# Kernel optimization log

Hardware: AMD Instinct MI355X
Metric: run time of the kernel (lower is better)

Reference implementation:

```python
import jax, jax.numpy as jnp
import numpy as np

HEADS = 16
HEAD_DIM = 64


def _attn(q, k, v):
    # q: [..., Q, h, d], k/v: [..., K, h, d]  (non-causal SDPA, scale 1/sqrt(d))
    scale = 1.0 / np.sqrt(HEAD_DIM).astype(np.float32)
    s = jnp.einsum('...qhd,...khd->...hqk', q, k) * scale
    p = jax.nn.softmax(s, axis=-1)
    return jnp.einsum('...hqk,...khd->...qhd', p, v)


def setup_inputs() -> dict:
    key = jax.random.key(0)
    k0, k1, k2 = jax.random.split(key, 3)
    B, T, H, W, D = 4, 32, 16, 16, 1024
    inner = HEADS * HEAD_DIM
    x = jax.random.normal(k0, (B, T, H, W, D), jnp.float32)
    Wqkv = jax.random.normal(k1, (D, 3 * inner), jnp.float32) / np.sqrt(D)
    Wout = jax.random.normal(k2, (inner, D), jnp.float32) / np.sqrt(inner)
    bout = jnp.zeros((D,), jnp.float32)
    return {"x": x, "Wqkv": Wqkv, "Wout": Wout, "bout": bout, "reference_length": 3}


def reference(x, Wqkv, Wout, bout, reference_length):
    B, T, H, W, D = x.shape
    length = reference_length + 1
    n = T // length            # n_frames (chunks)
    S = H * W                  # tokens per frame
    h, d = HEADS, HEAD_DIM

    qkv = jnp.einsum('bthwD,De->bthwe', x, Wqkv)
    q, k, v = jnp.split(qkv, 3, axis=-1)

    def rs(t):  # -> [B, n, length, S, h, d]
        return t.reshape(B, n, length, S, h, d)

    qr, kr, vr = rs(q), rs(k), rs(v)

    # non-last chunks: query = first frame of chunk, keys/values = remaining r frames
    q_pre = qr[:, :-1, 0]                                             # [B, n-1, S, h, d]
    k_pre = kr[:, :-1, 1:].reshape(B, n - 1, reference_length * S, h, d)
    v_pre = vr[:, :-1, 1:].reshape(B, n - 1, reference_length * S, h, d)
    o_pre = _attn(q_pre, k_pre, v_pre).reshape(B, n - 1, H, W, h * d)

    # last chunk: all `length` frames are queries, keys/values = frames 1..length-1
    q_last = qr[:, -1].reshape(B, length * S, h, d)
    k_last = kr[:, -1, 1:].reshape(B, reference_length * S, h, d)
    v_last = vr[:, -1, 1:].reshape(B, reference_length * S, h, d)
    o_last = _attn(q_last, k_last, v_last).reshape(B, length, H, W, h * d)

    o = jnp.concatenate([o_pre, o_last], axis=1)  # [B, n-1+length, H, W, inner]
    return jnp.einsum('bthwe,eD->bthwD', o, Wout) + bout
```

## Files before the change

kernel.cpp:

```cpp
#include <hip/hip_runtime.h>
#include <hip/hip_bf16.h>

typedef __bf16 bf16;
typedef __bf16 bf16x8 __attribute__((ext_vector_type(8)));
typedef float  f32x4  __attribute__((ext_vector_type(4)));
typedef float  f32x4v __attribute__((ext_vector_type(4)));
typedef unsigned int u32x4 __attribute__((ext_vector_type(4)));
typedef unsigned short u16x4 __attribute__((ext_vector_type(4)));

#define DEV __device__ __forceinline__

DEV void gload_lds16(const bf16* g, bf16* l) {
    __builtin_amdgcn_global_load_lds(
        (__attribute__((address_space(1))) void*)g,
        (__attribute__((address_space(3))) void*)l, 16, 0, 0);
}

DEV bf16x8 as_bf(u32x4 v) { return __builtin_bit_cast(bf16x8, v); }

DEV f32x4 mfma16(bf16x8 a, bf16x8 b, f32x4 c) {
    return __builtin_amdgcn_mfma_f32_16x16x32_bf16(a, b, c, 0, 0, 0);
}

DEV int cvtpk(float lo, float hi) {
    int r;
    asm("v_cvt_pk_bf16_f32 %0, %1, %2" : "=v"(r) : "v"(lo), "v"(hi));
    return r;
}

constexpr int D_   = 1024;
constexpr int S_   = 256;
constexpr int TOUT = 11;
constexpr int MQ   = 4 * TOUT * S_;
constexpr int MKV  = 4 * 8 * 3 * S_;
constexpr int KVL  = 768;

constexpr int PB_WQKV = 768;
constexpr int PB_WOUT = 256;
constexpr int PB_GQ   = MQ  * 128 / 256;
constexpr int PB_GKV  = MKV * 128 / 256;
constexpr int PB_TOT  = PB_WQKV + PB_WOUT + PB_GQ + PB_GKV;

__global__ void prep(const float* __restrict__ x,
                     const float* __restrict__ Wqkv,
                     const float* __restrict__ Wout,
                     bf16* __restrict__ Aq, bf16* __restrict__ Akv,
                     bf16* __restrict__ Wqkv_t, bf16* __restrict__ Wout_t)
{
    __shared__ float T[64][65];
    const int tid = threadIdx.x;
    int wg = blockIdx.x;

    if (wg < PB_WQKV + PB_WOUT) {
        const float* W; bf16* Wt; int N, bid2;
        if (wg < PB_WQKV) { W = Wqkv; Wt = Wqkv_t; N = 3072; bid2 = wg; }
        else              { W = Wout; Wt = Wout_t; N = 1024; bid2 = wg - PB_WQKV; }
        const int kt = bid2 & 15, nt = bid2 >> 4;
        const int k0 = kt * 64, n0 = nt * 64;
        for (int i = 0; i < 16; ++i) {
            const int e = i * 256 + tid;
            const int kk = e >> 6, nn = e & 63;
            T[nn][kk] = W[(size_t)(k0 + kk) * N + n0 + nn];
        }
        __syncthreads();
        for (int i = 0; i < 16; ++i) {
            const int e = i * 256 + tid;
            const int n = e >> 6, kk = e & 63;
            Wt[(size_t)(n0 + n) * 1024 + k0 + kk] = (bf16)T[n][kk];
        }
        return;
    }
    wg -= PB_WQKV + PB_WOUT;

    int row, part;
    const float* src;
    bf16* dst;
    if (wg < PB_GQ) {
        const int idx = wg * 256 + tid;
        row = idx >> 7; part = idx & 127;
        const int b    = row / (TOUT * S_);
        const int r2   = row - b * (TOUT * S_);
        const int tout = r2 >> 8;
        const int s    = r2 & 255;
        const int tx   = tout < 7 ? tout * 4 : 28 + (tout - 7);
        src = x + ((size_t)((b * 32 + tx) * S_ + s)) * D_ + part * 8;
        dst = Aq + (size_t)row * D_ + part * 8;
    } else {
        const int idx = (wg - PB_GQ) * 256 + tid;
        row = idx >> 7; part = idx & 127;
        const int b  = row / 6144;
        const int r2 = row - b * 6144;
        const int c  = r2 / KVL;
        const int j  = r2 - c * KVL;
        const int f  = 1 + (j >> 8);
        const int s  = j & 255;
        const int tx = c * 4 + f;
        src = x + ((size_t)((b * 32 + tx) * S_ + s)) * D_ + part * 8;
        dst = Akv + (size_t)row * D_ + part * 8;
    }
    f32x4v v0 = *(const f32x4v*)src;
    f32x4v v1 = *(const f32x4v*)(src + 4);
    bf16x8 o;
    o[0]=(bf16)v0[0]; o[1]=(bf16)v0[1]; o[2]=(bf16)v0[2]; o[3]=(bf16)v0[3];
    o[4]=(bf16)v1[0]; o[5]=(bf16)v1[1]; o[6]=(bf16)v1[2]; o[7]=(bf16)v1[3];
    *(bf16x8*)dst = o;
}

#define PH_BEGIN() do { \
    __builtin_amdgcn_s_barrier(); \
    asm volatile("s_waitcnt lgkmcnt(0)" ::: "memory"); \
    __builtin_amdgcn_sched_barrier(0); \
    __builtin_amdgcn_s_setprio(1); \
} while(0)

#define PH_MMEND() do { \
    __builtin_amdgcn_s_setprio(0); \
    __builtin_amdgcn_sched_barrier(0); \
} while(0)

#define PH_CLOSE4() do { \
    asm volatile("s_waitcnt vmcnt(4)" ::: "memory"); \
    __builtin_amdgcn_s_barrier(); \
} while(0)

#define STAGE_A(bufc, half, tile) do { \
    const bf16* s0_ = pA + (size_t)(half) * 64 * 1024 + (tile) * 64; \
    bf16* d0_ = ldsA + (bufc) * 16384 + (half) * 8192; \
    gload_lds16(s0_, d0_); \
    gload_lds16(s0_ + (size_t)128 * 1024, d0_ + 4096); \
} while(0)

#define STAGE_B(bufc, half, tile) do { \
    const bf16* s0_ = pB + (size_t)(half) * 32 * 1024 + (tile) * 64; \
    bf16* d0_ = ldsB + (bufc) * 16384 + (half) * 8192; \
    gload_lds16(s0_, d0_); \
    gload_lds16(s0_ + (size_t)128 * 1024, d0_ + 4096); \
} while(0)

#define LDAJ(dst, bufc, mh, J) do { \
    const bf16* p_ = sm + (bufc) * 16384 + (mh) * 8192 + (J) * 1024; \
    dst[J][0] = *(const u32x4*)(p_ + eA0); \
    dst[J][1] = *(const u32x4*)(p_ + eA1); \
} while(0)

#define LDBH(dst, bufc, nh) do { \
    const bf16* p_ = sm + 32768 + (bufc) * 16384 + (nh) * 8192; \
    dst[0][0] = *(const u32x4*)(p_ + eB0); \
    dst[0][1] = *(const u32x4*)(p_ + eB1); \
    dst[1][0] = *(const u32x4*)(p_ + 1024 + eB0); \
    dst[1][1] = *(const u32x4*)(p_ + 1024 + eB1); \
} while(0)

#define MMX(av, bv, mh, nh) do { \
    _Pragma("unroll") \
    for (int j_ = 0; j_ < 4; ++j_) { \
        _Pragma("unroll") \
        for (int i_ = 0; i_ < 2; ++i_) { \
            f32x4 c_ = acc[(mh)*4 + j_][(nh)*2 + i_]; \
            c_ = mfma16(as_bf(av[j_][0]), as_bf(bv[i_][0]), c_); \
            c_ = mfma16(as_bf(av[j_][1]), as_bf(bv[i_][1]), c_); \
            acc[(mh)*4 + j_][(nh)*2 + i_] = c_; \
        } \
    } \
} while(0)

#define GEMM_MAINLOOP() do { \
    STAGE_A(0, 0, 0); STAGE_A(0, 1, 0); STAGE_B(0, 0, 0); STAGE_B(0, 1, 0); \
    STAGE_A(1, 0, 1); STAGE_B(1, 0, 1); STAGE_B(1, 1, 1); \
    asm volatile("s_waitcnt vmcnt(0)" ::: "memory"); \
    __builtin_amdgcn_s_barrier(); \
    LDAJ(aX,0,0,0); LDAJ(aX,0,0,1); LDAJ(aX,0,0,2); LDAJ(aX,0,0,3); \
    LDBH(bP0,0,0); LDBH(bQ0,0,1); \
    _Pragma("unroll 1") \
    for (int t = 0; t < 8; ++t) { \
        const int T1 = 2 * t + 1; \
        const int n0 = (2 * t + 2 < 15) ? 2 * t + 2 : 15; \
        const int n1 = (2 * t + 3 < 15) ? 2 * t + 3 : 15; \
        STAGE_A(1, 1, T1); STAGE_B(0, 0, n0); \
        PH_BEGIN(); MMX(aX, bP0, 0, 0); MMX(aX, bQ0, 0, 1); PH_MMEND(); \
        LDAJ(aY, 0, 1, 0); LDAJ(aY, 0, 1, 1); LDAJ(aY, 0, 1, 2); LDAJ(aY, 0, 1, 3); \
        LDBH(bP1, 1, 0); \
        PH_CLOSE4(); \
        STAGE_A(0, 0, n0); STAGE_B(0, 1, n0); \
        PH_BEGIN(); MMX(aY, bP0, 1, 0); MMX(aY, bQ0, 1, 1); PH_MMEND(); \
        LDAJ(aX, 1, 0, 0); LDAJ(aX, 1, 0, 1); LDAJ(aX, 1, 0, 2); LDAJ(aX, 1, 0, 3); \
        LDBH(bQ1, 1, 1); \
        PH_CLOSE4(); \
        STAGE_A(0, 1, n0); STAGE_B(1, 0, n1); \
        PH_BEGIN(); MMX(aX, bP1, 0, 0); MMX(aX, bQ1, 0, 1); PH_MMEND(); \
        LDAJ(aY, 1, 1, 0); LDAJ(aY, 1, 1, 1); LDAJ(aY, 1, 1, 2); LDAJ(aY, 1, 1, 3); \
        LDBH(bP0, 0, 0); \
        PH_CLOSE4(); \
        STAGE_A(1, 0, n1); STAGE_B(1, 1, n1); \
        PH_BEGIN(); MMX(aY, bP1, 1, 0); MMX(aY, bQ1, 1, 1); PH_MMEND(); \
        LDAJ(aX, 0, 0, 0); LDAJ(aX, 0, 0, 1); LDAJ(aX, 0, 0, 2); LDAJ(aX, 0, 0, 3); \
        LDBH(bQ0, 0, 1); \
        PH_CLOSE4(); \
    } \
    asm volatile("s_waitcnt vmcnt(0) lgkmcnt(0)" ::: "memory"); \
} while(0)

#define GEMM_PREAMBLE() \
    const int wr = wid >> 2, wc = wid & 3; \
    const int l15 = lane & 15, l4 = lane >> 4; \
    const int Rrow = (wid << 3) + (lane >> 3); \
    const int G    = (lane & 7) ^ (lane >> 3); \
    const bf16* pA = A  + (size_t)(bm * 256 + Rrow) * 1024 + G * 8; \
    const int wc1 = Rrow >> 5, cc1 = Rrow & 31; \
    const bf16* pB = Bt + (size_t)(bn * 256 + wc1 * 64 + cc1) * 1024 + G * 8; \
    bf16* ldsA = sm + (wid << 9); \
    bf16* ldsB = sm + 32768 + (wid << 9); \
    const int g0  = l4 ^ (l15 & 7); \
    const int eA0 = wr * 4096 + l15 * 64 + g0 * 8; \
    const int eA1 = eA0 ^ 32; \
    const int eB0 = wc * 2048 + l15 * 64 + g0 * 8; \
    const int eB1 = eB0 ^ 32; \
    f32x4 acc[8][4]; \
    u32x4 aX[4][2], aY[4][2], bP0[2][2], bQ0[2][2], bP1[2][2], bQ1[2][2]; \
    { const f32x4 zf_ = {0.f, 0.f, 0.f, 0.f}; \
      _Pragma("unroll") \
      for (int m_ = 0; m_ < 8; ++m_) \
          _Pragma("unroll") \
          for (int n_ = 0; n_ < 4; ++n_) acc[m_][n_] = zf_; }

__global__ __launch_bounds__(512, 2) void gemm_qkv(
    const bf16* __restrict__ Aq, const bf16* __restrict__ Akv,
    const bf16* __restrict__ Wt,
    bf16* __restrict__ Qb, bf16* __restrict__ Kb, bf16* __restrict__ Vt)
{
    __shared__ bf16 sm[65536];
    const int tid = threadIdx.x, lane = tid & 63, wid = tid >> 6;

    int wg = blockIdx.x;
    {
        const int xcd = wg & 7, off = wg >> 3;
        wg = xcd * 118 + off;
    }
    const bool isQ = wg < 176;
    const bf16* A;  const bf16* Bt;  int bm, bn;
    if (isQ) {
        const int sg = wg >> 4, s = wg & 15;
        bm = sg * 4 + (s >> 2);
        bn = s & 3;
        A = Aq;  Bt = Wt;
    } else {
        const int id2 = wg - 176;
        const int sg = id2 >> 4, s = id2 & 15;
        bm = (sg % 24) * 4 + (s >> 2);
        bn = (sg / 24) * 4 + (s & 3);
        A = Akv; Bt = Wt + (size_t)1024 * 1024;
    }

    GEMM_PREAMBLE();
    GEMM_MAINLOOP();

    if (isQ || bn < 4) {
        bf16* C = isQ ? Qb : Kb;
        #pragma unroll
        for (int m = 0; m < 8; ++m) {
            const int row = bm * 256 + wr * 128 + m * 16 + l4 * 4;
            #pragma unroll
            for (int n = 0; n < 4; ++n) {
                const int col = bn * 256 + wc * 64 + n * 16 + l15;
                f32x4 v = acc[m][n];
                #pragma unroll
                for (int r = 0; r < 4; ++r)
                    C[(size_t)(row + r) * 1024 + col] = (bf16)v[r];
            }
        }
    } else {
        const int vb = bm / 3;
        const int j0base = (bm % 3) * 256;
        #pragma unroll
        for (int m = 0; m < 8; ++m) {
            const int j0 = j0base + wr * 128 + m * 16 + l4 * 4;
            #pragma unroll
            for (int n = 0; n < 4; ++n) {
                const int colv = (bn - 4) * 256 + wc * 64 + n * 16 + l15;
                f32x4 v = acc[m][n];
                u16x4 pk;
                #pragma unroll
                for (int r = 0; r < 4; ++r) {
                    bf16 t = (bf16)v[r];
                    pk[r] = __builtin_bit_cast(unsigned short, t);
                }
                *(u16x4*)(Vt + ((size_t)vb * 1024 + colv) * KVL + j0) = pk;
            }
        }
    }
}

__global__ __launch_bounds__(512, 2) void gemm_out(
    const bf16* __restrict__ A, const bf16* __restrict__ Bt,
    float* __restrict__ Cf, const float* __restrict__ bias)
{
    __shared__ bf16 sm[65536];
    const int tid = threadIdx.x, lane = tid & 63, wid = tid >> 6;

    int wg = blockIdx.x;
    {
        const int xcd = wg & 7, off = wg >> 3;
        wg = xcd * 22 + off;
    }
    const int sg = wg >> 4, s = wg & 15;
    const int bm = sg * 4 + (s >> 2), bn = s & 3;

    GEMM_PREAMBLE();
    GEMM_MAINLOOP();

    #pragma unroll
    for (int m = 0; m < 8; ++m) {
        const int row = bm * 256 + wr * 128 + m * 16 + l4 * 4;
        #pragma unroll
        for (int n = 0; n < 4; ++n) {
            const int col = bn * 256 + wc * 64 + n * 16 + l15;
            f32x4 v = acc[m][n];
            const float bs = bias[col];
            #pragma unroll
            for (int r = 0; r < 4; ++r)
                Cf[(size_t)(row + r) * 1024 + col] = v[r] + bs;
        }
    }
}

__global__ __launch_bounds__(256, 4) void attn_fwd(
    const bf16* __restrict__ Q, const bf16* __restrict__ K,
    const bf16* __restrict__ Vt, bf16* __restrict__ O)
{
    __shared__ bf16 Kl[2][2][64][32];
    __shared__ bf16 Vl[2][2][64][32];

    const int tid = threadIdx.x, lane = tid & 63, wid = tid >> 6;
    int bid = blockIdx.x;
    const int h = bid & 15; bid >>= 4;
    const int qt = bid % 44, b = bid / 44;
    const int chunk = qt < 28 ? (qt >> 2) : 7;
    const int qrow0 = b * (TOUT * S_) +
                      (qt < 28 ? chunk * S_ + (qt & 3) * 64 : 7 * S_ + (qt - 28) * 64);

    const bf16* kg = K  + ((size_t)(b * 8 + chunk) * KVL) * 1024 + h * 64;
    const bf16* vg = Vt + ((size_t)((b * 8 + chunk) * 16 + h)) * 64 * KVL;

    const int l15 = lane & 15, l4 = lane >> 4;

    const bf16* qp = Q + (size_t)(qrow0 + wid * 16 + l15) * D_ + h * 64 + l4 * 8;
    u32x4 q0, q1;
    {
        bf16x8 t0 = *(const bf16x8*)qp;
        bf16x8 t1 = *(const bf16x8*)(qp + 32);
        #pragma unroll
        for (int j = 0; j < 8; ++j) {
            t0[j] = (bf16)((float)t0[j] * 0.125f);
            t1[j] = (bf16)((float)t1[j] * 0.125f);
        }
        q0 = __builtin_bit_cast(u32x4, t0);
        q1 = __builtin_bit_cast(u32x4, t1);
    }

    const int R   = wid * 16 + (lane >> 2);
    const int gsw = ((lane & 3) ^ ((lane >> 3) & 3)) * 8;
    const int rg  = (l4 ^ ((l15 >> 1) & 3)) * 8;

    const int baseA = ((2 * (l4 & 1)) * 16 + l15) * 4;
    const int baseB = baseA + 64;
    const bool hi2 = (l4 & 2) != 0;

    float m_s = -1e30f, l_s = 0.f;
    f32x4 oacc[4];
    const f32x4 zf = {0.f, 0.f, 0.f, 0.f};
    #pragma unroll
    for (int m2 = 0; m2 < 4; ++m2) oacc[m2] = zf;

#define ASTAGE(c, t) do { \
    const int kv0_ = (t) * 64; \
    gload_lds16(kg + (size_t)(kv0_ + R) * 1024 + gsw,      &Kl[c][0][0][0] + wid * 512); \
    gload_lds16(kg + (size_t)(kv0_ + R) * 1024 + 32 + gsw, &Kl[c][1][0][0] + wid * 512); \
    gload_lds16(vg + (size_t)R * KVL + kv0_ + gsw,         &Vl[c][0][0][0] + wid * 512); \
    gload_lds16(vg + (size_t)R * KVL + kv0_ + 32 + gsw,    &Vl[c][1][0][0] + wid * 512); \
} while (0)

    ASTAGE(0, 0);
    __syncthreads();

    #pragma unroll 1
    for (int kt = 0; kt < 12; ++kt) {
        const int cur = kt & 1;
        if (kt < 11) ASTAGE(cur ^ 1, kt + 1);

        f32x4 s[4];
        #pragma unroll
        for (int n = 0; n < 4; ++n) {
            const bf16* kp = &Kl[cur][0][n * 16 + l15][0] + rg;
            const u32x4 k0 = *(const u32x4*)kp;
            const u32x4 k1 = *(const u32x4*)(kp + 2048);
            f32x4 t = mfma16(as_bf(k0), as_bf(q0), zf);
            s[n] = mfma16(as_bf(k1), as_bf(q1), t);
        }

        float pm = s[0][0];
        #pragma unroll
        for (int n = 0; n < 4; ++n)
            #pragma unroll
            for (int r = 0; r < 4; ++r) pm = fmaxf(pm, s[n][r]);
        pm = fmaxf(pm, __shfl_xor(pm, 16));
        pm = fmaxf(pm, __shfl_xor(pm, 32));
        const float mn = fmaxf(m_s, pm);
        const float al = __expf(m_s - mn);
        m_s = mn;
        float p[4][4];
        float sum = 0.f;
        #pragma unroll
        for (int n = 0; n < 4; ++n)
            #pragma unroll
            for (int r = 0; r < 4; ++r) {
                const float e = __expf(s[n][r] - mn);
                p[n][r] = e; sum += e;
            }
        sum += __shfl_xor(sum, 16);
        sum += __shfl_xor(sum, 32);
        l_s = l_s * al + sum;
        #pragma unroll
        for (int m2 = 0; m2 < 4; ++m2) oacc[m2] *= al;

        int u[4][2];
        #pragma unroll
        for (int n = 0; n < 4; ++n) {
            u[n][0] = cvtpk(p[n][0], p[n][1]);
            u[n][1] = cvtpk(p[n][2], p[n][3]);
        }

        #pragma unroll
        for (int kk = 0; kk < 2; ++kk) {
            const int e0 = __builtin_amdgcn_ds_bpermute(baseA, u[2 * kk][0]);
            const int f0 = __builtin_amdgcn_ds_bpermute(baseA, u[2 * kk + 1][0]);
            const int e1 = __builtin_amdgcn_ds_bpermute(baseA, u[2 * kk][1]);
            const int f1 = __builtin_amdgcn_ds_bpermute(baseA, u[2 * kk + 1][1]);
            const int e2 = __builtin_amdgcn_ds_bpermute(baseB, u[2 * kk][0]);
            const int f2 = __builtin_amdgcn_ds_bpermute(baseB, u[2 * kk + 1][0]);
            const int e3 = __builtin_amdgcn_ds_bpermute(baseB, u[2 * kk][1]);
            const int f3 = __builtin_amdgcn_ds_bpermute(baseB, u[2 * kk + 1][1]);
            u32x4 pb;
            pb[0] = (unsigned)(hi2 ? f0 : e0);
            pb[1] = (unsigned)(hi2 ? f1 : e1);
            pb[2] = (unsigned)(hi2 ? f2 : e2);
            pb[3] = (unsigned)(hi2 ? f3 : e3);
            #pragma unroll
            for (int m2 = 0; m2 < 4; ++m2) {
                const u32x4 vf = *(const u32x4*)(&Vl[cur][kk][m2 * 16 + l15][0] + rg);
                oacc[m2] = mfma16(as_bf(vf), as_bf(pb), oacc[m2]);
            }
        }
        __syncthreads();
    }
#undef ASTAGE

    const float inv = 1.f / l_s;
    bf16* sc = &Kl[0][0][0][0] + wid * 1152;
    #pragma unroll
    for (int m2 = 0; m2 < 4; ++m2)
        #pragma unroll
        for (int r = 0; r < 4; ++r)
            sc[l15 * 72 + m2 * 16 + l4 * 4 + r] = (bf16)(oacc[m2][r] * inv);
    const int rq = lane >> 2, rd = (lane & 3) * 16;
    const bf16* sr = sc + rq * 72 + rd;
    const u32x4 o0 = *(const u32x4*)sr;
    const u32x4 o1 = *(const u32x4*)(sr + 8);
    bf16* op = O + (size_t)(qrow0 + wid * 16 + rq) * D_ + h * 64 + rd;
    *(u32x4*)op = o0;
    *(u32x4*)(op + 8) = o1;
}

extern "C" void kernel_launch(void* const* d_in, const int* in_sizes, int n_in,
                              void* d_out, int out_size, void* d_ws, size_t ws_size,
                              hipStream_t stream) {
    (void)in_sizes; (void)n_in; (void)out_size; (void)ws_size;
    const float* x    = (const float*)d_in[0];
    const float* Wqkv = (const float*)d_in[1];
    const float* Wout = (const float*)d_in[2];
    const float* bout = (const float*)d_in[3];

    bf16* Aq     = (bf16*)d_ws;
    bf16* Akv    = Aq     + (size_t)MQ  * 1024;
    bf16* Wqkv_t = Akv    + (size_t)MKV * 1024;
    bf16* Wout_t = Wqkv_t + (size_t)3072 * 1024;
    bf16* Qb     = Wout_t + (size_t)1024 * 1024;
    bf16* Kb     = Qb     + (size_t)MQ  * 1024;
    bf16* Vtb    = Kb     + (size_t)MKV * 1024;
    bf16* Ob     = Aq;

    prep<<<PB_TOT, 256, 0, stream>>>(x, Wqkv, Wout, Aq, Akv, Wqkv_t, Wout_t);

    gemm_qkv<<<944, 512, 0, stream>>>(Aq, Akv, Wqkv_t, Qb, Kb, Vtb);

    attn_fwd<<<4 * 44 * 16, 256, 0, stream>>>(Qb, Kb, Vtb, Ob);

    gemm_out<<<176, 512, 0, stream>>>(Ob, Wout_t, (float*)d_out, bout);
}
```

Measured before the change: 285.1 us.

## Fuse fp32-to-bf16 activation gather into QKV GEMM A-operand loading

Removes the separate prep pass that gathered the x frames and converted them to bf16 into staging buffers. gemm_qkv now reads fp32 x directly, converts it in registers and writes bf16 tiles to LDS. The main loop is restructured into eight finer phases with a single set of B fragment registers and new vmcnt waits, and gemm_out gets the same reworked pipeline. This saves a full read and write of the activation matrix, at the cost of twice the global A traffic per GEMM tile plus extra VGPRs and conversion work inside the GEMM.

```diff
diff --git a/kernel.cpp b/kernel.cpp
--- a/kernel.cpp
+++ b/kernel.cpp
@@ -37,73 +37,31 @@
 
 constexpr int PB_WQKV = 768;
 constexpr int PB_WOUT = 256;
-constexpr int PB_GQ   = MQ  * 128 / 256;
-constexpr int PB_GKV  = MKV * 128 / 256;
-constexpr int PB_TOT  = PB_WQKV + PB_WOUT + PB_GQ + PB_GKV;
-
-__global__ void prep(const float* __restrict__ x,
-                     const float* __restrict__ Wqkv,
+
+__global__ void prep(const float* __restrict__ Wqkv,
                      const float* __restrict__ Wout,
-                     bf16* __restrict__ Aq, bf16* __restrict__ Akv,
                      bf16* __restrict__ Wqkv_t, bf16* __restrict__ Wout_t)
 {
     __shared__ float T[64][65];
     const int tid = threadIdx.x;
     int wg = blockIdx.x;
 
-    if (wg < PB_WQKV + PB_WOUT) {
-        const float* W; bf16* Wt; int N, bid2;
-        if (wg < PB_WQKV) { W = Wqkv; Wt = Wqkv_t; N = 3072; bid2 = wg; }
-        else              { W = Wout; Wt = Wout_t; N = 1024; bid2 = wg - PB_WQKV; }
-        const int kt = bid2 & 15, nt = bid2 >> 4;
-        const int k0 = kt * 64, n0 = nt * 64;
-        for (int i = 0; i < 16; ++i) {
-            const int e = i * 256 + tid;
-            const int kk = e >> 6, nn = e & 63;
-            T[nn][kk] = W[(size_t)(k0 + kk) * N + n0 + nn];
-        }
-        __syncthreads();
-        for (int i = 0; i < 16; ++i) {
-            const int e = i * 256 + tid;
-            const int n = e >> 6, kk = e & 63;
-            Wt[(size_t)(n0 + n) * 1024 + k0 + kk] = (bf16)T[n][kk];
-        }
-        return;
-    }
-    wg -= PB_WQKV + PB_WOUT;
-
-    int row, part;
-    const float* src;
-    bf16* dst;
-    if (wg < PB_GQ) {
-        const int idx = wg * 256 + tid;
-        row = idx >> 7; part = idx & 127;
-        const int b    = row / (TOUT * S_);
-        const int r2   = row - b * (TOUT * S_);
-        const int tout = r2 >> 8;
-        const int s    = r2 & 255;
-        const int tx   = tout < 7 ? tout * 4 : 28 + (tout - 7);
-        src = x + ((size_t)((b * 32 + tx) * S_ + s)) * D_ + part * 8;
-        dst = Aq + (size_t)row * D_ + part * 8;
-    } else {
-        const int idx = (wg - PB_GQ) * 256 + tid;
-        row = idx >> 7; part = idx & 127;
-        const int b  = row / 6144;
-        const int r2 = row - b * 6144;
-        const int c  = r2 / KVL;
-        const int j  = r2 - c * KVL;
-        const int f  = 1 + (j >> 8);
-        const int s  = j & 255;
-        const int tx = c * 4 + f;
-        src = x + ((size_t)((b * 32 + tx) * S_ + s)) * D_ + part * 8;
-        dst = Akv + (size_t)row * D_ + part * 8;
-    }
-    f32x4v v0 = *(const f32x4v*)src;
-    f32x4v v1 = *(const f32x4v*)(src + 4);
-    bf16x8 o;
-    o[0]=(bf16)v0[0]; o[1]=(bf16)v0[1]; o[2]=(bf16)v0[2]; o[3]=(bf16)v0[3];
-    o[4]=(bf16)v1[0]; o[5]=(bf16)v1[1]; o[6]=(bf16)v1[2]; o[7]=(bf16)v1[3];
-    *(bf16x8*)dst = o;
+    const float* W; bf16* Wt; int N, bid2;
+    if (wg < PB_WQKV) { W = Wqkv; Wt = Wqkv_t; N = 3072; bid2 = wg; }
+    else              { W = Wout; Wt = Wout_t; N = 1024; bid2 = wg - PB_WQKV; }
+    const int kt = bid2 & 15, nt = bid2 >> 4;
+    const int k0 = kt * 64, n0 = nt * 64;
+    for (int i = 0; i < 16; ++i) {
+        const int e = i * 256 + tid;
+        const int kk = e >> 6, nn = e & 63;
+        T[nn][kk] = W[(size_t)(k0 + kk) * N + n0 + nn];
+    }
+    __syncthreads();
+    for (int i = 0; i < 16; ++i) {
+        const int e = i * 256 + tid;
+        const int n = e >> 6, kk = e & 63;
+        Wt[(size_t)(n0 + n) * 1024 + k0 + kk] = (bf16)T[n][kk];
+    }
 }
 
 #define PH_BEGIN() do { \
@@ -118,8 +76,13 @@
     __builtin_amdgcn_sched_barrier(0); \
 } while(0)
 
-#define PH_CLOSE4() do { \
-    asm volatile("s_waitcnt vmcnt(4)" ::: "memory"); \
+#define PH_CLOSE() do { \
+    asm volatile("s_waitcnt vmcnt(6)" ::: "memory"); \
+    __builtin_amdgcn_s_barrier(); \
+} while(0)
+
+#define XCLOSE() do { \
+    asm volatile("s_waitcnt vmcnt(12)" ::: "memory"); \
     __builtin_amdgcn_s_barrier(); \
 } while(0)
 
@@ -135,6 +98,25 @@
     bf16* d0_ = ldsB + (bufc) * 16384 + (half) * 8192; \
     gload_lds16(s0_, d0_); \
     gload_lds16(s0_ + (size_t)128 * 1024, d0_ + 4096); \
+} while(0)
+
+#define ALD(set, half, tile) do { \
+    const float* s_ = px + (size_t)(half) * 65536 + (tile) * 64; \
+    set##0 = *(const f32x4v*)s_; \
+    set##1 = *(const f32x4v*)(s_ + 4); \
+    set##2 = *(const f32x4v*)(s_ + 131072); \
+    set##3 = *(const f32x4v*)(s_ + 131072 + 4); \
+} while(0)
+
+#define AWR(set, bufc, half) do { \
+    bf16* d_ = ldsA + (bufc) * 16384 + (half) * 8192 + lane * 8; \
+    bf16x8 o0_, o1_; \
+    o0_[0]=(bf16)set##0[0]; o0_[1]=(bf16)set##0[1]; o0_[2]=(bf16)set##0[2]; o0_[3]=(bf16)set##0[3]; \
+    o0_[4]=(bf16)set##1[0]; o0_[5]=(bf16)set##1[1]; o0_[6]=(bf16)set##1[2]; o0_[7]=(bf16)set##1[3]; \
+    o1_[0]=(bf16)set##2[0]; o1_[1]=(bf16)set##2[1]; o1_[2]=(bf16)set##2[2]; o1_[3]=(bf16)set##2[3]; \
+    o1_[4]=(bf16)set##3[0]; o1_[5]=(bf16)set##3[1]; o1_[6]=(bf16)set##3[2]; o1_[7]=(bf16)set##3[3]; \
+    *(bf16x8*)d_ = o0_; \
+    *(bf16x8*)(d_ + 4096) = o1_; \
 } while(0)
 
 #define LDAJ(dst, bufc, mh, J) do { \
@@ -164,48 +146,20 @@
     } \
 } while(0)
 
-#define GEMM_MAINLOOP() do { \
-    STAGE_A(0, 0, 0); STAGE_A(0, 1, 0); STAGE_B(0, 0, 0); STAGE_B(0, 1, 0); \
-    STAGE_A(1, 0, 1); STAGE_B(1, 0, 1); STAGE_B(1, 1, 1); \
-    asm volatile("s_waitcnt vmcnt(0)" ::: "memory"); \
-    __builtin_amdgcn_s_barrier(); \
-    LDAJ(aX,0,0,0); LDAJ(aX,0,0,1); LDAJ(aX,0,0,2); LDAJ(aX,0,0,3); \
-    LDBH(bP0,0,0); LDBH(bQ0,0,1); \
-    _Pragma("unroll 1") \
-    for (int t = 0; t < 8; ++t) { \
-        const int T1 = 2 * t + 1; \
-        const int n0 = (2 * t + 2 < 15) ? 2 * t + 2 : 15; \
-        const int n1 = (2 * t + 3 < 15) ? 2 * t + 3 : 15; \
-        STAGE_A(1, 1, T1); STAGE_B(0, 0, n0); \
-        PH_BEGIN(); MMX(aX, bP0, 0, 0); MMX(aX, bQ0, 0, 1); PH_MMEND(); \
-        LDAJ(aY, 0, 1, 0); LDAJ(aY, 0, 1, 1); LDAJ(aY, 0, 1, 2); LDAJ(aY, 0, 1, 3); \
-        LDBH(bP1, 1, 0); \
-        PH_CLOSE4(); \
-        STAGE_A(0, 0, n0); STAGE_B(0, 1, n0); \
-        PH_BEGIN(); MMX(aY, bP0, 1, 0); MMX(aY, bQ0, 1, 1); PH_MMEND(); \
-        LDAJ(aX, 1, 0, 0); LDAJ(aX, 1, 0, 1); LDAJ(aX, 1, 0, 2); LDAJ(aX, 1, 0, 3); \
-        LDBH(bQ1, 1, 1); \
-        PH_CLOSE4(); \
-        STAGE_A(0, 1, n0); STAGE_B(1, 0, n1); \
-        PH_BEGIN(); MMX(aX, bP1, 0, 0); MMX(aX, bQ1, 0, 1); PH_MMEND(); \
-        LDAJ(aY, 1, 1, 0); LDAJ(aY, 1, 1, 1); LDAJ(aY, 1, 1, 2); LDAJ(aY, 1, 1, 3); \
-        LDBH(bP0, 0, 0); \
-        PH_CLOSE4(); \
-        STAGE_A(1, 0, n1); STAGE_B(1, 1, n1); \
-        PH_BEGIN(); MMX(aY, bP1, 1, 0); MMX(aY, bQ1, 1, 1); PH_MMEND(); \
-        LDAJ(aX, 0, 0, 0); LDAJ(aX, 0, 0, 1); LDAJ(aX, 0, 0, 2); LDAJ(aX, 0, 0, 3); \
-        LDBH(bQ0, 0, 1); \
-        PH_CLOSE4(); \
-    } \
-    asm volatile("s_waitcnt vmcnt(0) lgkmcnt(0)" ::: "memory"); \
-} while(0)
-
-#define GEMM_PREAMBLE() \
+#define GEMM_REGS() \
+    f32x4 acc[8][4]; \
+    u32x4 aX[4][2], aY[4][2], bP[2][2], bQ[2][2]; \
+    { const f32x4 zf_ = {0.f, 0.f, 0.f, 0.f}; \
+      _Pragma("unroll") \
+      for (int m_ = 0; m_ < 8; ++m_) \
+          _Pragma("unroll") \
+          for (int n_ = 0; n_ < 4; ++n_) acc[m_][n_] = zf_; }
+
+#define GEMM_ADDR() \
     const int wr = wid >> 2, wc = wid & 3; \
     const int l15 = lane & 15, l4 = lane >> 4; \
     const int Rrow = (wid << 3) + (lane >> 3); \
     const int G    = (lane & 7) ^ (lane >> 3); \
-    const bf16* pA = A  + (size_t)(bm * 256 + Rrow) * 1024 + G * 8; \
     const int wc1 = Rrow >> 5, cc1 = Rrow & 31; \
     const bf16* pB = Bt + (size_t)(bn * 256 + wc1 * 64 + cc1) * 1024 + G * 8; \
     bf16* ldsA = sm + (wid << 9); \
@@ -214,18 +168,10 @@
     const int eA0 = wr * 4096 + l15 * 64 + g0 * 8; \
     const int eA1 = eA0 ^ 32; \
     const int eB0 = wc * 2048 + l15 * 64 + g0 * 8; \
-    const int eB1 = eB0 ^ 32; \
-    f32x4 acc[8][4]; \
-    u32x4 aX[4][2], aY[4][2], bP0[2][2], bQ0[2][2], bP1[2][2], bQ1[2][2]; \
-    { const f32x4 zf_ = {0.f, 0.f, 0.f, 0.f}; \
-      _Pragma("unroll") \
-      for (int m_ = 0; m_ < 8; ++m_) \
-          _Pragma("unroll") \
-          for (int n_ = 0; n_ < 4; ++n_) acc[m_][n_] = zf_; }
+    const int eB1 = eB0 ^ 32;
 
 __global__ __launch_bounds__(512, 2) void gemm_qkv(
-    const bf16* __restrict__ Aq, const bf16* __restrict__ Akv,
-    const bf16* __restrict__ Wt,
+    const float* __restrict__ x, const bf16* __restrict__ Wt,
     bf16* __restrict__ Qb, bf16* __restrict__ Kb, bf16* __restrict__ Vt)
 {
     __shared__ bf16 sm[65536];
@@ -237,22 +183,79 @@
         wg = xcd * 118 + off;
     }
     const bool isQ = wg < 176;
-    const bf16* A;  const bf16* Bt;  int bm, bn;
+    const bf16* Bt;  int bm, bn, xrow;
     if (isQ) {
         const int sg = wg >> 4, s = wg & 15;
-        bm = sg * 4 + (s >> 2);
-        bn = s & 3;
-        A = Aq;  Bt = Wt;
+        bm = sg * 4 + (s >> 2); bn = s & 3;
+        Bt = Wt;
+        const int b = bm / 11, tout = bm % 11;
+        const int tx = tout < 7 ? tout * 4 : 28 + (tout - 7);
+        xrow = (b * 32 + tx) * 256;
     } else {
         const int id2 = wg - 176;
-        const int sg = id2 >> 4, s = id2 & 15;
-        bm = (sg % 24) * 4 + (s >> 2);
-        bn = (sg / 24) * 4 + (s & 3);
-        A = Akv; Bt = Wt + (size_t)1024 * 1024;
-    }
-
-    GEMM_PREAMBLE();
-    GEMM_MAINLOOP();
+        const int sg = id2 >> 5, s = id2 & 31;
+        bm = sg * 4 + (s >> 3); bn = s & 7;
+        Bt = Wt + (size_t)1024 * 1024;
+        const int b = bm / 24, r2 = bm % 24, c = r2 / 3, part = r2 % 3;
+        const int tx = c * 4 + 1 + part;
+        xrow = (b * 32 + tx) * 256;
+    }
+
+    GEMM_ADDR();
+    const float* px = x + (size_t)(xrow + Rrow) * 1024 + G * 8;
+    GEMM_REGS();
+    f32x4v sX0, sX1, sX2, sX3, sY0, sY1, sY2, sY3;
+
+    ALD(sX, 0, 0);
+    ALD(sY, 1, 0);
+    STAGE_B(0, 0, 0); STAGE_B(0, 1, 0); STAGE_B(1, 0, 1); STAGE_B(1, 1, 1);
+    AWR(sX, 0, 0); AWR(sY, 0, 1);
+    ALD(sX, 0, 1);
+    AWR(sX, 1, 0);
+    ALD(sY, 1, 1);
+    asm volatile("s_waitcnt lgkmcnt(0)" ::: "memory");
+    __builtin_amdgcn_s_barrier();
+    LDAJ(aX,0,0,0); LDAJ(aX,0,0,1); LDAJ(aX,0,0,2); LDAJ(aX,0,0,3);
+    LDBH(bP,0,0);
+
+    #pragma unroll 1
+    for (int t = 0; t < 8; ++t) {
+        const int n0 = (2 * t + 2 < 15) ? 2 * t + 2 : 15;
+        const int n1 = (2 * t + 3 < 15) ? 2 * t + 3 : 15;
+        ALD(sX, 0, n0); AWR(sY, 1, 1);
+        PH_BEGIN(); MMX(aX, bP, 0, 0); PH_MMEND();
+        LDBH(bQ, 0, 1); LDAJ(aY, 0, 1, 0);
+        XCLOSE();
+        ALD(sY, 1, n0); AWR(sX, 0, 0);
+        PH_BEGIN(); MMX(aX, bQ, 0, 1); PH_MMEND();
+        LDAJ(aY, 0, 1, 1); LDAJ(aY, 0, 1, 2); LDAJ(aY, 0, 1, 3);
+        XCLOSE();
+        STAGE_B(0, 0, n0);
+        PH_BEGIN(); MMX(aY, bP, 1, 0); PH_MMEND();
+        LDAJ(aX, 1, 0, 0); LDAJ(aX, 1, 0, 1); LDAJ(aX, 1, 0, 2);
+        XCLOSE();
+        STAGE_B(0, 1, n0);
+        PH_BEGIN(); MMX(aY, bQ, 1, 1); PH_MMEND();
+        LDAJ(aX, 1, 0, 3); LDBH(bP, 1, 0);
+        XCLOSE();
+        ALD(sX, 0, n1); AWR(sY, 0, 1);
+        PH_BEGIN(); MMX(aX, bP, 0, 0); PH_MMEND();
+        LDBH(bQ, 1, 1); LDAJ(aY, 1, 1, 0);
+        XCLOSE();
+        ALD(sY, 1, n1); AWR(sX, 1, 0);
+        PH_BEGIN(); MMX(aX, bQ, 0, 1); PH_MMEND();
+        LDAJ(aY, 1, 1, 1); LDAJ(aY, 1, 1, 2); LDAJ(aY, 1, 1, 3);
+        XCLOSE();
+        STAGE_B(1, 0, n1);
+        PH_BEGIN(); MMX(aY, bP, 1, 0); PH_MMEND();
+        LDAJ(aX, 0, 0, 0); LDAJ(aX, 0, 0, 1); LDAJ(aX, 0, 0, 2);
+        XCLOSE();
+        STAGE_B(1, 1, n1);
+        PH_BEGIN(); MMX(aY, bQ, 1, 1); PH_MMEND();
+        LDAJ(aX, 0, 0, 3); LDBH(bP, 0, 0);
+        XCLOSE();
+    }
+    asm volatile("s_waitcnt vmcnt(0) lgkmcnt(0)" ::: "memory");
 
     if (isQ || bn < 4) {
         bf16* C = isQ ? Qb : Kb;
@@ -281,8 +284,8 @@
                 u16x4 pk;
                 #pragma unroll
                 for (int r = 0; r < 4; ++r) {
-                    bf16 t = (bf16)v[r];
-                    pk[r] = __builtin_bit_cast(unsigned short, t);
+                    bf16 tt = (bf16)v[r];
+                    pk[r] = __builtin_bit_cast(unsigned short, tt);
                 }
                 *(u16x4*)(Vt + ((size_t)vb * 1024 + colv) * KVL + j0) = pk;
             }
@@ -305,8 +308,55 @@
     const int sg = wg >> 4, s = wg & 15;
     const int bm = sg * 4 + (s >> 2), bn = s & 3;
 
-    GEMM_PREAMBLE();
-    GEMM_MAINLOOP();
+    GEMM_ADDR();
+    const bf16* pA = A + (size_t)(bm * 256 + Rrow) * 1024 + G * 8;
+    GEMM_REGS();
+
+    STAGE_A(0, 0, 0); STAGE_A(0, 1, 0); STAGE_B(0, 0, 0); STAGE_B(0, 1, 0);
+    STAGE_A(1, 0, 1); STAGE_B(1, 0, 1); STAGE_B(1, 1, 1);
+    asm volatile("s_waitcnt vmcnt(6)" ::: "memory");
+    __builtin_amdgcn_s_barrier();
+    LDAJ(aX,0,0,0); LDAJ(aX,0,0,1); LDAJ(aX,0,0,2); LDAJ(aX,0,0,3);
+    LDBH(bP,0,0);
+    #pragma unroll 1
+    for (int t = 0; t < 8; ++t) {
+        const int T1 = 2 * t + 1;
+        const int n0 = (2 * t + 2 < 15) ? 2 * t + 2 : 15;
+        const int n1 = (2 * t + 3 < 15) ? 2 * t + 3 : 15;
+        STAGE_A(1, 1, T1);
+        PH_BEGIN(); MMX(aX, bP, 0, 0); PH_MMEND();
+        LDBH(bQ, 0, 1); LDAJ(aY, 0, 1, 0);
+        PH_CLOSE();
+        STAGE_A(0, 0, n0);
+        PH_BEGIN(); MMX(aX, bQ, 0, 1); PH_MMEND();
+        LDAJ(aY, 0, 1, 1); LDAJ(aY, 0, 1, 2); LDAJ(aY, 0, 1, 3);
+        PH_CLOSE();
+        STAGE_B(0, 0, n0);
+        PH_BEGIN(); MMX(aY, bP, 1, 0); PH_MMEND();
+        LDAJ(aX, 1, 0, 0); LDAJ(aX, 1, 0, 1); LDAJ(aX, 1, 0, 2);
+        PH_CLOSE();
+        STAGE_B(0, 1, n0);
+        PH_BEGIN(); MMX(aY, bQ, 1, 1); PH_MMEND();
+        LDAJ(aX, 1, 0, 3); LDBH(bP, 1, 0);
+        PH_CLOSE();
+        STAGE_A(0, 1, n0);
+        PH_BEGIN(); MMX(aX, bP, 0, 0); PH_MMEND();
+        LDBH(bQ, 1, 1); LDAJ(aY, 1, 1, 0);
+        PH_CLOSE();
+        STAGE_A(1, 0, n1);
+        PH_BEGIN(); MMX(aX, bQ, 0, 1); PH_MMEND();
+        LDAJ(aY, 1, 1, 1); LDAJ(aY, 1, 1, 2); LDAJ(aY, 1, 1, 3);
+        PH_CLOSE();
+        STAGE_B(1, 0, n1);
+        PH_BEGIN(); MMX(aY, bP, 1, 0); PH_MMEND();
+        LDAJ(aX, 0, 0, 0); LDAJ(aX, 0, 0, 1); LDAJ(aX, 0, 0, 2);
+        PH_CLOSE();
+        STAGE_B(1, 1, n1);
+        PH_BEGIN(); MMX(aY, bQ, 1, 1); PH_MMEND();
+        LDAJ(aX, 0, 0, 3); LDBH(bP, 0, 0);
+        PH_CLOSE();
+    }
+    asm volatile("s_waitcnt vmcnt(0) lgkmcnt(0)" ::: "memory");
 
     #pragma unroll
     for (int m = 0; m < 8; ++m) {
@@ -479,18 +529,16 @@
     const float* Wout = (const float*)d_in[2];
     const float* bout = (const float*)d_in[3];
 
-    bf16* Aq     = (bf16*)d_ws;
-    bf16* Akv    = Aq     + (size_t)MQ  * 1024;
-    bf16* Wqkv_t = Akv    + (size_t)MKV * 1024;
+    bf16* Ob     = (bf16*)d_ws;
+    bf16* Wqkv_t = Ob     + (size_t)(MQ + MKV) * 1024;
     bf16* Wout_t = Wqkv_t + (size_t)3072 * 1024;
     bf16* Qb     = Wout_t + (size_t)1024 * 1024;
     bf16* Kb     = Qb     + (size_t)MQ  * 1024;
     bf16* Vtb    = Kb     + (size_t)MKV * 1024;
-    bf16* Ob     = Aq;
-
-    prep<<<PB_TOT, 256, 0, stream>>>(x, Wqkv, Wout, Aq, Akv, Wqkv_t, Wout_t);
-
-    gemm_qkv<<<944, 512, 0, stream>>>(Aq, Akv, Wqkv_t, Qb, Kb, Vtb);
+
+    prep<<<PB_WQKV + PB_WOUT, 256, 0, stream>>>(Wqkv, Wout, Wqkv_t, Wout_t);
+
+    gemm_qkv<<<944, 512, 0, stream>>>(x, Wqkv_t, Qb, Kb, Vtb);
 
     attn_fwd<<<4 * 44 * 16, 256, 0, stream>>>(Qb, Kb, Vtb, Ob);
 
```

Result: slower. 313.4 us, median of 2 (+9.9%).
